# Kernel tuning notes

Hardware: AMD Instinct MI355X
Metric: run time of the kernel (lower is better)

## Reference

```python
import jax, jax.numpy as jnp
import numpy as np
from jax import lax

B_BLK = 16   # block size B
N_Z = 64     # latent dim


def setup_inputs() -> dict:
    key = jax.random.key(0)
    ks = jax.random.split(key, 6)
    in_ch, out_ch = 256, 256
    L = (out_ch // B_BLK) * (in_ch // B_BLK)  # 256 latent codes
    x = jax.random.normal(ks[0], (32, in_ch, 64, 64), dtype=jnp.float32)
    z = jax.random.normal(ks[1], (L, N_Z), dtype=jnp.float32)
    W1 = jax.random.normal(ks[2], (B_BLK, N_Z, N_Z), dtype=jnp.float32) * 0.1
    B1 = jax.random.normal(ks[3], (B_BLK, N_Z), dtype=jnp.float32) * 0.1
    W2 = jax.random.normal(ks[4], (B_BLK, B_BLK * 9, N_Z), dtype=jnp.float32) * 0.1
    B2 = jax.random.normal(ks[5], (B_BLK, B_BLK * 9), dtype=jnp.float32) * 0.1
    return {"x": x, "z": z, "W1": W1, "B1": B1, "W2": W2, "B2": B2}


def _aggregate_weight(z, W1, B1, W2, B2, out_ch, in_ch):
    # hypertype='separate', batched over all L = (out_ch//B)*(in_ch//B) blocks.
    # per block: a = W1 @ z + B1 -> (B, N_z); K = W2 @ a[...,None] + B2 -> (B, B*9)
    a = jnp.einsum('bdn,ln->lbd', W1, z) + B1            # (L, B, N_z)
    K = jnp.einsum('bkd,lbd->lbk', W2, a) + B2           # (L, B, B*9)
    ob, ib = out_ch // B_BLK, in_ch // B_BLK
    K = K.reshape(ob, ib, B_BLK, B_BLK, 3, 3)            # (o_blk, i_blk, b1, b2, 3, 3)
    # torch: K.reshape(B,B,3,3).permute(1,0,2,3) => weight_block[p,q] = K[q,p]
    # then cat over i_blk on dim 1 (in), over o_blk on dim 0 (out)
    w = K.transpose(0, 3, 1, 2, 4, 5)                    # (o_blk, b2, i_blk, b1, 3, 3)
    return w.reshape(out_ch, in_ch, 3, 3)


def reference(x, z, W1, B1, W2, B2):
    out_ch, in_ch = 256, 256
    weight = _aggregate_weight(z, W1, B1, W2, B2, out_ch, in_ch)
    # F.conv2d(x, weight, bias=None, stride=1, padding=kernel_size//2=1)
    return lax.conv_general_dilated(
        x, weight,
        window_strides=(1, 1),
        padding=[(1, 1), (1, 1)],
        dimension_numbers=('NCHW', 'OIHW', 'NCHW'))
```

## Files before the change

kernel.cpp:

```cpp
#include <hip/hip_runtime.h>

typedef unsigned short u16;
typedef unsigned int u32;
typedef __attribute__((ext_vector_type(8))) short short8;
typedef __attribute__((ext_vector_type(4))) float f32x4;

__device__ __forceinline__ u16 f2bf(float f) {
    u32 u = __float_as_uint(f);
    return (u16)((u + 0x7FFFu + ((u >> 16) & 1u)) >> 16);
}

__global__ __launch_bounds__(256) void nchw2nhwc(const float* __restrict__ x,
                                                 u16* __restrict__ xb) {
    __shared__ float tile[64][65];
    const int b   = blockIdx.x;
    const int n   = b >> 8;
    const int icb = (b >> 6) & 3;
    const int pxb = b & 63;
    const int ic0 = icb * 64, px0 = pxb * 64;

    const int g = threadIdx.x >> 6, lx = threadIdx.x & 63;
    const float* src = x + (size_t)(n * 256 + ic0) * 4096 + px0 + lx;
#pragma unroll
    for (int r = 0; r < 16; ++r) {
        int row = g * 16 + r;
        tile[row][lx] = src[(size_t)row * 4096];
    }
    __syncthreads();
    const int tp = threadIdx.x & 31, pz = threadIdx.x >> 5;
    u16* dst = xb + ((size_t)(n * 4096) + px0) * 256 + ic0 + tp * 2;
#pragma unroll
    for (int r = 0; r < 8; ++r) {
        int p = pz * 8 + r;
        u32 pv = ((u32)f2bf(tile[tp * 2 + 1][p]) << 16) | f2bf(tile[tp * 2][p]);
        *(u32*)(dst + (size_t)p * 256) = pv;
    }
}

__global__ __launch_bounds__(256) void wgen(const float* __restrict__ z,
                                            const float* __restrict__ W1,
                                            const float* __restrict__ B1,
                                            const float* __restrict__ W2,
                                            const float* __restrict__ B2,
                                            u16* __restrict__ wb) {
    __shared__ float zl[64];
    __shared__ float aL[1024];
    const int l = blockIdx.x;
    const int tid = threadIdx.x;
    if (tid < 64) zl[tid] = z[l * 64 + tid];
    __syncthreads();
#pragma unroll
    for (int i = 0; i < 4; ++i) {
        int idx = i * 256 + tid;
        const float* wrow = W1 + (size_t)idx * 64;
        float s = B1[idx];
        for (int nn = 0; nn < 64; ++nn) s += wrow[nn] * zl[nn];
        aL[idx] = s;
    }
    __syncthreads();
    const int b1 = tid >> 4, b2 = tid & 15;
    const int ob = l >> 4, ib = l & 15;
    const int ic = ib * 16 + b1;
    const int oc = ob * 16 + b2;
    const size_t wbase = (size_t)oc * 2304 + (size_t)(ic >> 5) * 288 + (ic & 31);
    const float* arow = aL + b1 * 64;
#pragma unroll
    for (int tap = 0; tap < 9; ++tap) {
        int kk = b2 * 9 + tap;
        const float* w2row = W2 + (size_t)(b1 * 144 + kk) * 64;
        float s = B2[b1 * 144 + kk];
        for (int d = 0; d < 64; ++d) s += w2row[d] * arow[d];
        wb[wbase + tap * 32] = f2bf(s);
    }
}

__global__ __launch_bounds__(256) void conv_mfma(const u16* __restrict__ xb,
                                                 const u16* __restrict__ wb,
                                                 float* __restrict__ out) {
    __shared__ __align__(16) u16 As[128 * 32];
    __shared__ __align__(16) u16 Bs[128 * 32];

    const int tid = threadIdx.x;
    const int bid = blockIdx.x;
    const int mt = bid & 1;
    const int nt = bid >> 1;
    const int n = nt >> 5;
    const int pimg = (nt & 31) << 7;
    const int oc0 = mt << 7;

    const int lane = tid & 63;
    const int wave = tid >> 6;
    const int wm = (wave >> 1) & 1, wn = wave & 1;
    const int lr = lane & 15, lq = lane >> 4;

    const int qa = tid, qb = tid + 256;
    const int r0 = qa >> 2, c0 = qa & 3;
    const int r1 = qb >> 2, c1 = qb & 3;

    const u16* aw0 = wb + (size_t)(oc0 + r0) * 2304 + c0 * 8;
    const u16* aw1 = wb + (size_t)(oc0 + r1) * 2304 + c1 * 8;
    u16* asw0 = As + r0 * 32 + c0 * 8;
    u16* asw1 = As + r1 * 32 + c1 * 8;

    const int po0 = pimg + r0, po1 = pimg + r1;
    const int ho0 = po0 >> 6, wo0 = po0 & 63;
    const int ho1 = po1 >> 6, wo1 = po1 & 63;
    const u16* bx0 = xb + ((size_t)n * 4096 + po0) * 256 + c0 * 8;
    const u16* bx1 = xb + ((size_t)n * 4096 + po1) * 256 + c1 * 8;
    u16* bsw0 = Bs + r0 * 32 + c0 * 8;
    u16* bsw1 = Bs + r1 * 32 + c1 * 8;

    f32x4 acc[4][4];
    const f32x4 z4 = {0.f, 0.f, 0.f, 0.f};
#pragma unroll
    for (int i = 0; i < 4; ++i)
#pragma unroll
        for (int j = 0; j < 4; ++j) acc[i][j] = z4;

    int icb = 0, tap = 0;
    for (int kt = 0; kt < 72; ++kt) {
        const int dh = tap / 3 - 1, dw = tap % 3 - 1;
        const int goff = (dh * 64 + dw) * 256 + icb * 32;
        const int aoffk = kt * 32;

        uint4 av0 = *(const uint4*)(aw0 + aoffk);
        uint4 av1 = *(const uint4*)(aw1 + aoffk);
        uint4 bv0 = {0, 0, 0, 0}, bv1 = {0, 0, 0, 0};
        {
            int hi = ho0 + dh, wi = wo0 + dw;
            if ((unsigned)hi < 64u && (unsigned)wi < 64u)
                bv0 = *(const uint4*)(bx0 + goff);
        }
        {
            int hi = ho1 + dh, wi = wo1 + dw;
            if ((unsigned)hi < 64u && (unsigned)wi < 64u)
                bv1 = *(const uint4*)(bx1 + goff);
        }
        *(uint4*)asw0 = av0;
        *(uint4*)asw1 = av1;
        *(uint4*)bsw0 = bv0;
        *(uint4*)bsw1 = bv1;
        __syncthreads();

        short8 af[4], bf[4];
#pragma unroll
        for (int i = 0; i < 4; ++i) {
            af[i] = *(const short8*)(As + (wm * 64 + i * 16 + lr) * 32 + lq * 8);
            bf[i] = *(const short8*)(Bs + (wn * 64 + i * 16 + lr) * 32 + lq * 8);
        }
#pragma unroll
        for (int i = 0; i < 4; ++i)
#pragma unroll
            for (int j = 0; j < 4; ++j)
                acc[i][j] = __builtin_amdgcn_mfma_f32_16x16x32_bf16(
                    af[i], bf[j], acc[i][j], 0, 0, 0);
        __syncthreads();
        if (++tap == 9) { tap = 0; ++icb; }
    }

    const size_t outn = (size_t)n * 256 * 4096;
#pragma unroll
    for (int i = 0; i < 4; ++i) {
        int ocb = oc0 + wm * 64 + i * 16 + lq * 4;
#pragma unroll
        for (int j = 0; j < 4; ++j) {
            int po = pimg + wn * 64 + j * 16 + lr;
            float* op = out + outn + (size_t)ocb * 4096 + po;
#pragma unroll
            for (int r = 0; r < 4; ++r) op[(size_t)r * 4096] = acc[i][j][r];
        }
    }
}

extern "C" void kernel_launch(void* const* d_in, const int* in_sizes, int n_in,
                              void* d_out, int out_size, void* d_ws, size_t ws_size,
                              hipStream_t stream) {
    const float* x  = (const float*)d_in[0];
    const float* z  = (const float*)d_in[1];
    const float* W1 = (const float*)d_in[2];
    const float* B1 = (const float*)d_in[3];
    const float* W2 = (const float*)d_in[4];
    const float* B2 = (const float*)d_in[5];
    float* out = (float*)d_out;

    u16* xb = (u16*)d_ws;
    u16* wb = xb + (size_t)32 * 4096 * 256;
    const size_t need = ((size_t)32 * 4096 * 256 + (size_t)256 * 2304) * 2;
    if (ws_size < need) return;

    nchw2nhwc<<<dim3(8192), dim3(256), 0, stream>>>(x, xb);
    wgen<<<dim3(256), dim3(256), 0, stream>>>(z, W1, B1, W2, B2, wb);
    conv_mfma<<<dim3(2048), dim3(256), 0, stream>>>(xb, wb, out);
}
```

Before: 457.1 us.

## Pad NHWC input, double-buffer LDS via direct global-to-LDS loads with swizzle

The input conversion now writes a zero-padded 66x66 NHWC bf16 buffer, which removes per-load bounds checks in the conv kernel. The conv kernel double-buffers its A and B tiles in shared memory and fills them with global_load_lds 16-byte direct copies, using an XOR swizzle to avoid LDS bank conflicts. The weight layout is reordered to tap-major with K stepping tap then channel block, and block IDs are remapped for better L2 locality. The padded buffer costs extra workspace and border-zeroing writes, and the pipeline relies on a single barrier per iteration being enough for correctness.

New measurement: 448.8 us. No clear change (-1.8%).

```diff
diff --git a/kernel.cpp b/kernel.cpp
--- a/kernel.cpp
+++ b/kernel.cpp
@@ -10,30 +10,65 @@
     return (u16)((u + 0x7FFFu + ((u >> 16) & 1u)) >> 16);
 }
 
-__global__ __launch_bounds__(256) void nchw2nhwc(const float* __restrict__ x,
-                                                 u16* __restrict__ xb) {
-    __shared__ float tile[64][65];
+__device__ __forceinline__ void gld16(const u16* g, u16* l) {
+    __builtin_amdgcn_global_load_lds(
+        (const __attribute__((address_space(1))) unsigned int*)(unsigned long long)(const void*)g,
+        (__attribute__((address_space(3))) unsigned int*)(unsigned long long)(void*)l,
+        16, 0, 0);
+}
+
+__global__ __launch_bounds__(256) void nchw2nhwc_pad(const float* __restrict__ x,
+                                                     u16* __restrict__ xp) {
+    __shared__ float tile[64][66];
+    const int tid = threadIdx.x;
     const int b   = blockIdx.x;
     const int n   = b >> 8;
     const int icb = (b >> 6) & 3;
-    const int pxb = b & 63;
-    const int ic0 = icb * 64, px0 = pxb * 64;
-
-    const int g = threadIdx.x >> 6, lx = threadIdx.x & 63;
-    const float* src = x + (size_t)(n * 256 + ic0) * 4096 + px0 + lx;
-#pragma unroll
-    for (int r = 0; r < 16; ++r) {
-        int row = g * 16 + r;
-        tile[row][lx] = src[(size_t)row * 4096];
+    const int row = b & 63;
+    const int ic0 = icb * 64;
+
+    const int q = tid & 15, r0 = tid >> 4;
+    const float* src = x + (size_t)(n * 256 + ic0) * 4096 + row * 64 + q * 4;
+#pragma unroll
+    for (int rr = 0; rr < 4; ++rr) {
+        const int r = r0 + rr * 16;
+        const float4 v = *(const float4*)(src + (size_t)r * 4096);
+        float2* t0 = (float2*)&tile[r][q * 4];
+        t0[0] = make_float2(v.x, v.y);
+        t0[1] = make_float2(v.z, v.w);
     }
     __syncthreads();
-    const int tp = threadIdx.x & 31, pz = threadIdx.x >> 5;
-    u16* dst = xb + ((size_t)(n * 4096) + px0) * 256 + ic0 + tp * 2;
-#pragma unroll
-    for (int r = 0; r < 8; ++r) {
-        int p = pz * 8 + r;
-        u32 pv = ((u32)f2bf(tile[tp * 2 + 1][p]) << 16) | f2bf(tile[tp * 2][p]);
-        *(u32*)(dst + (size_t)p * 256) = pv;
+
+    const int c = tid & 7, ph = tid >> 3;
+    u16* dst = xp + ((size_t)n * 4356 + (size_t)(row + 1) * 66 + 1) * 256 + ic0 + c * 8;
+#pragma unroll
+    for (int pp = 0; pp < 2; ++pp) {
+        const int p = ph + pp * 32;
+        u32 w0[4];
+#pragma unroll
+        for (int k = 0; k < 4; ++k) {
+            const float f0 = tile[c * 8 + 2 * k][p];
+            const float f1 = tile[c * 8 + 2 * k + 1][p];
+            w0[k] = ((u32)f2bf(f1) << 16) | f2bf(f0);
+        }
+        uint4 v4; v4.x = w0[0]; v4.y = w0[1]; v4.z = w0[2]; v4.w = w0[3];
+        *(uint4*)(dst + (size_t)p * 256) = v4;
+    }
+
+    u16* hrow = xp + ((size_t)n * 4356 + (size_t)(row + 1) * 66) * 256 + ic0;
+    if (tid < 64) {
+        const int wp = (tid >> 5) ? 65 : 0;
+        *(u32*)(hrow + (size_t)wp * 256 + (tid & 31) * 2) = 0u;
+    }
+    if (row == 0) {
+        u16* tb = xp + (size_t)n * 4356 * 256 + ic0;
+        for (int i = tid; i < 2112; i += 256)
+            *(u32*)(tb + (size_t)(i >> 5) * 256 + (i & 31) * 2) = 0u;
+    }
+    if (row == 63) {
+        u16* bb = xp + ((size_t)n * 4356 + 65 * 66) * 256 + ic0;
+        for (int i = tid; i < 2112; i += 256)
+            *(u32*)(bb + (size_t)(i >> 5) * 256 + (i & 31) * 2) = 0u;
     }
 }
 
@@ -62,7 +97,7 @@
     const int ob = l >> 4, ib = l & 15;
     const int ic = ib * 16 + b1;
     const int oc = ob * 16 + b2;
-    const size_t wbase = (size_t)oc * 2304 + (size_t)(ic >> 5) * 288 + (ic & 31);
+    const size_t wbase = (size_t)oc * 2304 + ic;
     const float* arow = aL + b1 * 64;
 #pragma unroll
     for (int tap = 0; tap < 9; ++tap) {
@@ -70,18 +105,19 @@
         const float* w2row = W2 + (size_t)(b1 * 144 + kk) * 64;
         float s = B2[b1 * 144 + kk];
         for (int d = 0; d < 64; ++d) s += w2row[d] * arow[d];
-        wb[wbase + tap * 32] = f2bf(s);
-    }
-}
-
-__global__ __launch_bounds__(256) void conv_mfma(const u16* __restrict__ xb,
+        wb[wbase + (size_t)tap * 256] = f2bf(s);
+    }
+}
+
+__global__ __launch_bounds__(256) void conv_mfma(const u16* __restrict__ xp,
                                                  const u16* __restrict__ wb,
                                                  float* __restrict__ out) {
-    __shared__ __align__(16) u16 As[128 * 32];
-    __shared__ __align__(16) u16 Bs[128 * 32];
+    __shared__ __align__(16) u16 As[2][128 * 32];
+    __shared__ __align__(16) u16 Bs[2][128 * 32];
 
     const int tid = threadIdx.x;
-    const int bid = blockIdx.x;
+    const int b0  = blockIdx.x;
+    const int bid = (b0 & 7) * 256 + (b0 >> 3);
     const int mt = bid & 1;
     const int nt = bid >> 1;
     const int n = nt >> 5;
@@ -92,23 +128,32 @@
     const int wave = tid >> 6;
     const int wm = (wave >> 1) & 1, wn = wave & 1;
     const int lr = lane & 15, lq = lane >> 4;
-
-    const int qa = tid, qb = tid + 256;
-    const int r0 = qa >> 2, c0 = qa & 3;
-    const int r1 = qb >> 2, c1 = qb & 3;
-
-    const u16* aw0 = wb + (size_t)(oc0 + r0) * 2304 + c0 * 8;
-    const u16* aw1 = wb + (size_t)(oc0 + r1) * 2304 + c1 * 8;
-    u16* asw0 = As + r0 * 32 + c0 * 8;
-    u16* asw1 = As + r1 * 32 + c1 * 8;
-
-    const int po0 = pimg + r0, po1 = pimg + r1;
-    const int ho0 = po0 >> 6, wo0 = po0 & 63;
-    const int ho1 = po1 >> 6, wo1 = po1 & 63;
-    const u16* bx0 = xb + ((size_t)n * 4096 + po0) * 256 + c0 * 8;
-    const u16* bx1 = xb + ((size_t)n * 4096 + po1) * 256 + c1 * 8;
-    u16* bsw0 = Bs + r0 * 32 + c0 * 8;
-    u16* bsw1 = Bs + r1 * 32 + c1 * 8;
+    const int sw = (lq ^ (lr & 3)) * 8;
+
+    const int ls = lane >> 2;
+    const int swst = ((lane & 3) ^ (ls & 3)) * 8;
+    const int rr0 = wave * 32 + ls;
+    const int rr1 = rr0 + 16;
+    const u16* wbA0 = wb + (size_t)(oc0 + rr0) * 2304 + swst;
+    const u16* wbA1 = wb + (size_t)(oc0 + rr1) * 2304 + swst;
+    const int p0 = pimg + rr0, p1 = pimg + rr1;
+    const int pb0 = ((p0 >> 6) + 1) * 66 + (p0 & 63) + 1;
+    const int pb1 = ((p1 >> 6) + 1) * 66 + (p1 & 63) + 1;
+    const u16* xpN = xp + (size_t)n * 4356 * 256 + swst;
+
+    auto stage = [&](int bi, int kt) {
+        const int tap = kt >> 3, icb = kt & 7;
+        const int t3 = tap / 3;
+        const int dh = t3 - 1, dw = tap - t3 * 3 - 1;
+        const int ko = tap * 256 + icb * 32;
+        const int bo = (dh * 66 + dw) * 256 + icb * 32;
+        u16* ab = &As[bi][wave * 1024];
+        u16* bb = &Bs[bi][wave * 1024];
+        gld16(wbA0 + ko, ab);
+        gld16(wbA1 + ko, ab + 512);
+        gld16(xpN + (pb0 * 256 + bo), bb);
+        gld16(xpN + (pb1 * 256 + bo), bb + 512);
+    };
 
     f32x4 acc[4][4];
     const f32x4 z4 = {0.f, 0.f, 0.f, 0.f};
@@ -117,36 +162,20 @@
 #pragma unroll
         for (int j = 0; j < 4; ++j) acc[i][j] = z4;
 
-    int icb = 0, tap = 0;
+    stage(0, 0);
+#pragma unroll 2
     for (int kt = 0; kt < 72; ++kt) {
-        const int dh = tap / 3 - 1, dw = tap % 3 - 1;
-        const int goff = (dh * 64 + dw) * 256 + icb * 32;
-        const int aoffk = kt * 32;
-
-        uint4 av0 = *(const uint4*)(aw0 + aoffk);
-        uint4 av1 = *(const uint4*)(aw1 + aoffk);
-        uint4 bv0 = {0, 0, 0, 0}, bv1 = {0, 0, 0, 0};
-        {
-            int hi = ho0 + dh, wi = wo0 + dw;
-            if ((unsigned)hi < 64u && (unsigned)wi < 64u)
-                bv0 = *(const uint4*)(bx0 + goff);
-        }
-        {
-            int hi = ho1 + dh, wi = wo1 + dw;
-            if ((unsigned)hi < 64u && (unsigned)wi < 64u)
-                bv1 = *(const uint4*)(bx1 + goff);
-        }
-        *(uint4*)asw0 = av0;
-        *(uint4*)asw1 = av1;
-        *(uint4*)bsw0 = bv0;
-        *(uint4*)bsw1 = bv1;
+        const int cur = kt & 1;
         __syncthreads();
-
+        if (kt < 71) stage(cur ^ 1, kt + 1);
+
+        const u16* Ab = &As[cur][0];
+        const u16* Bb = &Bs[cur][0];
         short8 af[4], bf[4];
 #pragma unroll
         for (int i = 0; i < 4; ++i) {
-            af[i] = *(const short8*)(As + (wm * 64 + i * 16 + lr) * 32 + lq * 8);
-            bf[i] = *(const short8*)(Bs + (wn * 64 + i * 16 + lr) * 32 + lq * 8);
+            af[i] = *(const short8*)(Ab + (wm * 64 + i * 16 + lr) * 32 + sw);
+            bf[i] = *(const short8*)(Bb + (wn * 64 + i * 16 + lr) * 32 + sw);
         }
 #pragma unroll
         for (int i = 0; i < 4; ++i)
@@ -154,17 +183,15 @@
             for (int j = 0; j < 4; ++j)
                 acc[i][j] = __builtin_amdgcn_mfma_f32_16x16x32_bf16(
                     af[i], bf[j], acc[i][j], 0, 0, 0);
-        __syncthreads();
-        if (++tap == 9) { tap = 0; ++icb; }
     }
 
     const size_t outn = (size_t)n * 256 * 4096;
 #pragma unroll
     for (int i = 0; i < 4; ++i) {
-        int ocb = oc0 + wm * 64 + i * 16 + lq * 4;
+        const int ocb = oc0 + wm * 64 + i * 16 + lq * 4;
 #pragma unroll
         for (int j = 0; j < 4; ++j) {
-            int po = pimg + wn * 64 + j * 16 + lr;
+            const int po = pimg + wn * 64 + j * 16 + lr;
             float* op = out + outn + (size_t)ocb * 4096 + po;
 #pragma unroll
             for (int r = 0; r < 4; ++r) op[(size_t)r * 4096] = acc[i][j][r];
@@ -183,12 +210,12 @@
     const float* B2 = (const float*)d_in[5];
     float* out = (float*)d_out;
 
-    u16* xb = (u16*)d_ws;
-    u16* wb = xb + (size_t)32 * 4096 * 256;
-    const size_t need = ((size_t)32 * 4096 * 256 + (size_t)256 * 2304) * 2;
+    u16* xp = (u16*)d_ws;
+    u16* wb = xp + (size_t)32 * 4356 * 256;
+    const size_t need = ((size_t)32 * 4356 * 256 + (size_t)256 * 2304) * 2;
     if (ws_size < need) return;
 
-    nchw2nhwc<<<dim3(8192), dim3(256), 0, stream>>>(x, xb);
+    nchw2nhwc_pad<<<dim3(8192), dim3(256), 0, stream>>>(x, xp);
     wgen<<<dim3(256), dim3(256), 0, stream>>>(z, W1, B1, W2, B2, wb);
-    conv_mfma<<<dim3(2048), dim3(256), 0, stream>>>(xb, wb, out);
-}
+    conv_mfma<<<dim3(2048), dim3(256), 0, stream>>>(xp, wb, out);
+}
```
